# Performance work log

Measured on AMD Instinct MI355X. Metric: run time of the kernel, lower is better.

The kernel has to match this reference:

```python
import jax, jax.numpy as jnp
import numpy as np

WIDTH = 64
HEIGHT = 64
FEAT = 128
LAT = 64
NUM_SLOTS = 7


def pixel_coords(img_size):
    g = jnp.linspace(-1.0, 1.0, img_size)
    g1, g2 = jnp.meshgrid(g, g, indexing='ij')  # matches torch.meshgrid default
    return jnp.stack([g1, g2], axis=0)[None]  # (1, 2, S, S)


def clamp_pg(x, lo, hi):
    # clamp that preserves gradients (straight-through)
    return x + jax.lax.stop_gradient(jnp.clip(x, lo, hi) - x)


def setup_inputs() -> dict:
    key = jax.random.key(0)
    k0, k1, k2, k3 = jax.random.split(key, 4)
    bs = 64
    x = jax.random.normal(k0, (bs, FEAT, WIDTH, HEIGHT), jnp.float32)
    rand_pixel = jax.random.uniform(k1, (bs, 1, WIDTH, HEIGHT), jnp.float32)
    conv_w = jax.random.normal(k2, (LAT, FEAT), jnp.float32) / np.sqrt(FEAT)
    conv_b = jax.random.normal(k3, (LAT,), jnp.float32) * 0.01
    gate = jnp.asarray(0.5, jnp.float32)  # ScalarGate parameter (nonzero so c_f is non-degenerate)
    # laplacian kernel: sigma_init = 1 / (sqrt(num_slots) * log 2)
    log_sigma = jnp.asarray(np.log(1.0 / (np.sqrt(NUM_SLOTS) * np.log(2.0))), jnp.float32)
    return {'x': x, 'rand_pixel': rand_pixel, 'conv_w': conv_w, 'conv_b': conv_b,
            'gate': gate, 'log_sigma': log_sigma, 'num_cl_steps': 6}


def _forward(x, rand_pixel, conv_w, conv_b, gate, log_sigma, num_cl_steps):
    bs = x.shape[0]
    # SemiConv: gated 1x1 conv + fixed uv coordinate channels
    out = gate * (jnp.einsum('of,bfhw->bohw', conv_w, x) + conv_b[None, :, None, None])
    uv = jnp.concatenate([jnp.zeros((1, LAT - 2, WIDTH, HEIGHT), out.dtype),
                          pixel_coords(WIDTH).astype(out.dtype)], axis=1)
    c_f = out + uv                      # (bs, LAT, W, H)
    delta = out[:, -2:]                 # (bs, 2, W, H)
    sigma = jnp.exp(log_sigma)
    c_flat = c_f.reshape(bs, LAT, -1)   # (bs, LAT, W*H)
    b_idx = jnp.arange(bs)
    log_s0 = jnp.zeros((bs, 1, WIDTH, HEIGHT), c_f.dtype)

    def step(log_s, _):
        # interpolate-to-same-size is identity -> scope = exp(log_s)
        probs = (rand_pixel * jnp.exp(log_s)).reshape(bs, -1)
        idx = jnp.argmax(probs, axis=1)                 # (bs,)
        seed = c_flat[b_idx, :, idx]                    # (bs, LAT)
        diff = c_f - seed[:, :, None, None]
        dist = jnp.sqrt(clamp_pg((diff ** 2).sum(1), 1e-10, 1e10))  # euclidian (laplacian kernel)
        alpha = jnp.exp(-dist / sigma)[:, None]         # (bs, 1, W, H)
        alpha = clamp_pg(alpha, 0.01, 0.99)
        log_m = log_s + jnp.log(alpha)
        new_log_s = log_s + jnp.log1p(-alpha)
        return new_log_s, (log_m, new_log_s, seed)

    log_s_final, (log_m_steps, log_s_steps, seeds) = jax.lax.scan(
        step, log_s0, None, length=num_cl_steps)
    # log_m_k has num_cl_steps masks plus the final scope appended
    log_m_k = jnp.concatenate([log_m_steps, log_s_final[None]], axis=0)
    log_s_k = jnp.concatenate([log_s0[None], log_s_steps], axis=0)
    return log_m_k, log_s_k, c_f, delta, seeds


def reference(x, rand_pixel, conv_w, conv_b, gate, log_sigma, num_cl_steps):
    return _forward(x, rand_pixel, conv_w, conv_b, gate, log_sigma, num_cl_steps)
```

## Files before the change

kernel.cpp:

```cpp
#include <hip/hip_runtime.h>
#include <hip/hip_bf16.h>

#define NPIX 4096
#define FEAT 128
#define LAT 64
#define BS 64
#define NSTEPS 6

#define OFF_LOGM  0u
#define OFF_LOGS  1835008u
#define OFF_CF    3670016u
#define OFF_DELTA 20447232u
#define OFF_SEEDS 20971520u

typedef float f32x4 __attribute__((ext_vector_type(4)));
typedef short s16x8 __attribute__((ext_vector_type(8)));

__device__ __forceinline__ void amax_comb(float& bv, int& bi, float v, int i) {
    if (v > bv || (v == bv && i < bi)) { bv = v; bi = i; }
}

__device__ __forceinline__ short f2bf_rne(float r) {
    __hip_bfloat16 h = __float2bfloat16(r);
    return __builtin_bit_cast(short, h);
}

__device__ __forceinline__ void split2(float v, short& hi, short& lo) {
    unsigned u = __builtin_bit_cast(unsigned, v);
    hi = (short)(u >> 16);
    float hf = __builtin_bit_cast(float, u & 0xFFFF0000u);
    lo = f2bf_rne(v - hf);
}

__device__ __forceinline__ void transpose4(float4& v, int b) {
    float4 w;
    w.x = __shfl_xor(v.x, 1, 64); w.y = __shfl_xor(v.y, 1, 64);
    w.z = __shfl_xor(v.z, 1, 64); w.w = __shfl_xor(v.w, 1, 64);
    float4 u;
    if ((b & 1) == 0) u = make_float4(v.x, w.x, v.z, w.z);
    else              u = make_float4(w.y, v.y, w.w, v.w);
    float4 w2;
    w2.x = __shfl_xor(u.x, 2, 64); w2.y = __shfl_xor(u.y, 2, 64);
    w2.z = __shfl_xor(u.z, 2, 64); w2.w = __shfl_xor(u.w, 2, 64);
    if ((b & 2) == 0) v = make_float4(u.x, u.y, w2.x, w2.y);
    else              v = make_float4(w2.z, w2.w, u.z, u.w);
}

__global__ void prep_w(const float* __restrict__ w, const float* __restrict__ gate_p,
                       short* __restrict__ gwh, short* __restrict__ gwl)
{
    int i = blockIdx.x * 256 + threadIdx.x;
    float v = gate_p[0] * w[i];
    short h, l; split2(v, h, l);
    gwh[i] = h; gwl[i] = l;
}

__global__ __launch_bounds__(512, 2) void conv_mfma(
    const float* __restrict__ x, const float* __restrict__ rand_pixel,
    const float* __restrict__ bias, const float* __restrict__ gate_p,
    float* __restrict__ out,
    float* __restrict__ pval, int* __restrict__ pidx, int* __restrict__ cnt,
    const short* __restrict__ gwh, const short* __restrict__ gwl)
{
    __shared__ __align__(16) short Xhi[256][40];
    __shared__ __align__(16) short Xlo[256][40];
    __shared__ __align__(16) short Whi[64][132];
    __shared__ __align__(16) short Wlo[64][132];
    __shared__ float sbias[64];

    const int tid  = threadIdx.x;
    const int b    = blockIdx.x >> 4;
    const int tile = blockIdx.x & 15;
    const int p0   = tile * 256;
    const int lane = tid & 63;
    const int wv   = tid >> 6;
    const int l15  = lane & 15;
    const int lg   = lane >> 4;
    const int oh   = wv >> 2;
    const int pxq  = wv & 3;

    const int q  = tid >> 2;
    const int j  = tid & 3;
    const int P  = (q & 63) * 4;
    const int g0 = q >> 6;

    if (tile == 0 && tid < 8) cnt[b * 8 + tid] = 0;
    if (tid < 64) sbias[tid] = gate_p[0] * bias[tid];

    const float* xb = x + (size_t)b * FEAT * NPIX + p0;
    float4 v[4][4];
    #pragma unroll
    for (int kc = 0; kc < 4; ++kc)
        #pragma unroll
        for (int i = 0; i < 4; ++i) {
            int g = g0 + 2 * i;
            v[kc][i] = *(const float4*)(xb + (size_t)(kc * 32 + g * 4 + j) * NPIX + P);
        }

    {
        const int o = tid >> 3, c = (tid & 7) * 16;
        *(s16x8*)&Whi[o][c]     = *(const s16x8*)&gwh[o * 128 + c];
        *(s16x8*)&Whi[o][c + 8] = *(const s16x8*)&gwh[o * 128 + c + 8];
        *(s16x8*)&Wlo[o][c]     = *(const s16x8*)&gwl[o * 128 + c];
        *(s16x8*)&Wlo[o][c + 8] = *(const s16x8*)&gwl[o * 128 + c + 8];
    }

    #pragma unroll
    for (int i = 0; i < 4; ++i) {
        int g = g0 + 2 * i;
        float4 t = v[0][i]; transpose4(t, j);
        short h0, l0, h1, l1, h2, l2, h3, l3;
        split2(t.x, h0, l0); split2(t.y, h1, l1);
        split2(t.z, h2, l2); split2(t.w, h3, l3);
        *(short4*)&Xhi[P + j][g * 4] = make_short4(h0, h1, h2, h3);
        *(short4*)&Xlo[P + j][g * 4] = make_short4(l0, l1, l2, l3);
    }
    __syncthreads();

    f32x4 acc[2][4];
    #pragma unroll
    for (int og2 = 0; og2 < 2; ++og2)
        #pragma unroll
        for (int pg = 0; pg < 4; ++pg)
            acc[og2][pg] = (f32x4){0.f, 0.f, 0.f, 0.f};

    #pragma unroll
    for (int kc = 0; kc < 4; ++kc) {
        s16x8 Ah[2], Al[2];
        #pragma unroll
        for (int og2 = 0; og2 < 2; ++og2) {
            int o = oh * 32 + og2 * 16 + l15;
            Ah[og2] = *(const s16x8*)&Whi[o][kc * 32 + lg * 8];
            Al[og2] = *(const s16x8*)&Wlo[o][kc * 32 + lg * 8];
        }

        #pragma unroll
        for (int pg = 0; pg < 4; ++pg) {
            int pxl = pxq * 64 + pg * 16 + l15;
            s16x8 Bh = *(const s16x8*)&Xhi[pxl][lg * 8];
            s16x8 Bl = *(const s16x8*)&Xlo[pxl][lg * 8];
            #pragma unroll
            for (int og2 = 0; og2 < 2; ++og2) {
                acc[og2][pg] = __builtin_amdgcn_mfma_f32_16x16x32_bf16(Ah[og2], Bh, acc[og2][pg], 0, 0, 0);
                acc[og2][pg] = __builtin_amdgcn_mfma_f32_16x16x32_bf16(Ah[og2], Bl, acc[og2][pg], 0, 0, 0);
                acc[og2][pg] = __builtin_amdgcn_mfma_f32_16x16x32_bf16(Al[og2], Bh, acc[og2][pg], 0, 0, 0);
            }
        }

        if (kc < 3) {
            __syncthreads();
            #pragma unroll
            for (int i = 0; i < 4; ++i) {
                int g = g0 + 2 * i;
                float4 t = v[kc + 1][i]; transpose4(t, j);
                short h0, l0, h1, l1, h2, l2, h3, l3;
                split2(t.x, h0, l0); split2(t.y, h1, l1);
                split2(t.z, h2, l2); split2(t.w, h3, l3);
                *(short4*)&Xhi[P + j][g * 4] = make_short4(h0, h1, h2, h3);
                *(short4*)&Xlo[P + j][g * 4] = make_short4(l0, l1, l2, l3);
            }
            __syncthreads();
        }
    }

    float* cf = out + OFF_CF + (size_t)b * LAT * NPIX;
    #pragma unroll
    for (int og2 = 0; og2 < 2; ++og2) {
        #pragma unroll
        for (int pg = 0; pg < 4; ++pg) {
            #pragma unroll
            for (int r = 0; r < 4; ++r) {
                int o = oh * 32 + og2 * 16 + lg * 4 + r;
                int p = p0 + pxq * 64 + pg * 16 + l15;
                float vv = acc[og2][pg][r] + sbias[o];
                if (o == 62) {
                    out[OFF_DELTA + ((size_t)b * 2 + 0) * NPIX + p] = vv;
                    vv += (float)(-1.0 + 2.0 * (double)(p >> 6) / 63.0);
                } else if (o == 63) {
                    out[OFF_DELTA + ((size_t)b * 2 + 1) * NPIX + p] = vv;
                    vv += (float)(-1.0 + 2.0 * (double)(p & 63) / 63.0);
                }
                cf[(size_t)o * NPIX + p] = vv;
            }
        }
    }

    if (wv == 0) {
        *(float4*)(out + OFF_LOGS + (size_t)b * NPIX + p0 + lane * 4) =
            make_float4(0.f, 0.f, 0.f, 0.f);
        float4 rv = *(const float4*)(rand_pixel + (size_t)b * NPIX + p0 + lane * 4);
        int pb = p0 + lane * 4;
        float bv = rv.x; int bi = pb;
        if (rv.y > bv) { bv = rv.y; bi = pb + 1; }
        if (rv.z > bv) { bv = rv.z; bi = pb + 2; }
        if (rv.w > bv) { bv = rv.w; bi = pb + 3; }
        #pragma unroll
        for (int off = 32; off > 0; off >>= 1) {
            float ov = __shfl_down(bv, off, 64);
            int   oi = __shfl_down(bi, off, 64);
            amax_comb(bv, bi, ov, oi);
        }
        if (lane == 0) { pval[blockIdx.x] = bv; pidx[blockIdx.x] = bi; }
    }
}

#define REP16(OP) OP(0) OP(1) OP(2) OP(3) OP(4) OP(5) OP(6) OP(7) \
                  OP(8) OP(9) OP(10) OP(11) OP(12) OP(13) OP(14) OP(15)

__global__ __launch_bounds__(1024, 4) void steps_fused(
    const float* __restrict__ rand_pixel, const float* __restrict__ log_sigma_p,
    float* __restrict__ out, float* pv, int* pi, int* cnt)
{
    __shared__ float s_mv[16];
    __shared__ int   s_mi[16];
    __shared__ __align__(16) float s_seed[LAT];
    __shared__ float s_rv[16];
    __shared__ int   s_ri[16];

    const int tid  = threadIdx.x;
    const int b    = blockIdx.x >> 2;
    const int tile = blockIdx.x & 3;
    const int p    = tile * 1024 + tid;

    const float* cfb = out + OFF_CF + (size_t)b * LAT * NPIX;

#define DECLR(i) f32x4 r##i;
    REP16(DECLR)
#define LOADR(i) r##i = (f32x4){ cfb[(size_t)(4*i+0)*NPIX + p], cfb[(size_t)(4*i+1)*NPIX + p], \
                                 cfb[(size_t)(4*i+2)*NPIX + p], cfb[(size_t)(4*i+3)*NPIX + p] };
    REP16(LOADR)

    f32x4 aq = r0 * r0;
#define SQR(i) aq += r##i * r##i;
    SQR(1) SQR(2) SQR(3) SQR(4) SQR(5) SQR(6) SQR(7)
    SQR(8) SQR(9) SQR(10) SQR(11) SQR(12) SQR(13) SQR(14) SQR(15)
    const float cr2 = aq[0] + aq[1] + aq[2] + aq[3];

    const float rp    = rand_pixel[(size_t)b * NPIX + p];
    const float sigma = expf(log_sigma_p[0]);
    float ls = 0.f;

    #pragma unroll 1
    for (int s = 0; s < NSTEPS; ++s) {
        if (s > 0) {
            if (tid == 0) {
                while (__hip_atomic_load(&cnt[b * 8 + s], __ATOMIC_ACQUIRE,
                                         __HIP_MEMORY_SCOPE_AGENT) < 4)
                    __builtin_amdgcn_s_sleep(2);
            }
            __syncthreads();
        }
        const int nmerge = (s == 0) ? 16 : 4;
        if (tid < nmerge) {
            s_mv[tid] = __hip_atomic_load(&pv[(s * BS + b) * 16 + tid],
                                          __ATOMIC_RELAXED, __HIP_MEMORY_SCOPE_AGENT);
            s_mi[tid] = __hip_atomic_load(&pi[(s * BS + b) * 16 + tid],
                                          __ATOMIC_RELAXED, __HIP_MEMORY_SCOPE_AGENT);
        }
        __syncthreads();

        float bv = -1.0f; int bi = 0;
        for (int k = 0; k < nmerge; ++k) amax_comb(bv, bi, s_mv[k], s_mi[k]);

        if (tid < LAT) s_seed[tid] = cfb[(size_t)tid * NPIX + bi];
        __syncthreads();
        if (tile == 0 && tid < LAT)
            out[OFF_SEEDS + ((size_t)s * BS + b) * LAT + tid] = s_seed[tid];

        f32x4 dacc = (f32x4){0.f, 0.f, 0.f, 0.f};
        f32x4 sacc = (f32x4){0.f, 0.f, 0.f, 0.f};
#define DOT(i) { f32x4 sv = *(const f32x4*)&s_seed[4*i]; dacc += r##i * sv; sacc += sv * sv; }
        REP16(DOT)
        float dot = dacc[0] + dacc[1] + dacc[2] + dacc[3];
        float s2  = sacc[0] + sacc[1] + sacc[2] + sacc[3];
        float d2  = cr2 + s2 - 2.0f * dot;

        float dist  = sqrtf(fminf(fmaxf(d2, 1e-10f), 1e10f));
        float alpha = expf(-dist / sigma);
        alpha = fminf(fmaxf(alpha, 0.01f), 0.99f);
        float lm  = ls + logf(alpha);
        float lsn = ls + log1pf(-alpha);

        out[OFF_LOGM + ((size_t)s * BS + b) * NPIX + p]       = lm;
        out[OFF_LOGS + ((size_t)(s + 1) * BS + b) * NPIX + p] = lsn;
        ls = lsn;

        if (s == NSTEPS - 1) {
            out[OFF_LOGM + ((size_t)NSTEPS * BS + b) * NPIX + p] = lsn;
        } else {
            float prob = rp * expf(lsn);
            int   idx  = p;
            #pragma unroll
            for (int off = 32; off > 0; off >>= 1) {
                float ov = __shfl_down(prob, off, 64);
                int   oi = __shfl_down(idx, off, 64);
                amax_comb(prob, idx, ov, oi);
            }
            int lane = tid & 63, wid = tid >> 6;
            if (lane == 0) { s_rv[wid] = prob; s_ri[wid] = idx; }
            __syncthreads();
            if (tid == 0) {
                float fb = s_rv[0]; int fi = s_ri[0];
                #pragma unroll
                for (int k = 1; k < 16; ++k) amax_comb(fb, fi, s_rv[k], s_ri[k]);
                __hip_atomic_store(&pv[((s + 1) * BS + b) * 16 + tile], fb,
                                   __ATOMIC_RELAXED, __HIP_MEMORY_SCOPE_AGENT);
                __hip_atomic_store(&pi[((s + 1) * BS + b) * 16 + tile], fi,
                                   __ATOMIC_RELAXED, __HIP_MEMORY_SCOPE_AGENT);
                __hip_atomic_fetch_add(&cnt[b * 8 + s + 1], 1,
                                       __ATOMIC_RELEASE, __HIP_MEMORY_SCOPE_AGENT);
            }
        }
    }
}

__global__ __launch_bounds__(1024, 4) void step_kernel(
    const float* __restrict__ rand_pixel, const float* __restrict__ log_sigma_p,
    float* __restrict__ out, float* pv, int* pi, int step)
{
    __shared__ float s_mv[16];
    __shared__ int   s_mi[16];
    __shared__ __align__(16) float s_seed[LAT];
    __shared__ float s_rv[16];
    __shared__ int   s_ri[16];

    const int tid  = threadIdx.x;
    const int b    = blockIdx.x >> 2;
    const int tile = blockIdx.x & 3;
    const int p    = tile * 1024 + tid;

    const float* cfb = out + OFF_CF + (size_t)b * LAT * NPIX;

    const int nmerge = (step == 0) ? 16 : 4;
    if (tid < nmerge) { s_mv[tid] = pv[(step * BS + b) * 16 + tid];
                        s_mi[tid] = pi[(step * BS + b) * 16 + tid]; }
    __syncthreads();
    float bv = -1.0f; int bi = 0;
    for (int k = 0; k < nmerge; ++k) amax_comb(bv, bi, s_mv[k], s_mi[k]);

    if (tid < LAT) s_seed[tid] = cfb[(size_t)tid * NPIX + bi];
    __syncthreads();
    if (tile == 0 && tid < LAT)
        out[OFF_SEEDS + ((size_t)step * BS + b) * LAT + tid] = s_seed[tid];

    float d2 = 0.f;
    #pragma unroll
    for (int c = 0; c < LAT; ++c) {
        float d = cfb[(size_t)c * NPIX + p] - s_seed[c];
        d2 = fmaf(d, d, d2);
    }
    float dist  = sqrtf(fminf(fmaxf(d2, 1e-10f), 1e10f));
    float sigma = expf(log_sigma_p[0]);
    float alpha = expf(-dist / sigma);
    alpha = fminf(fmaxf(alpha, 0.01f), 0.99f);

    float ls  = out[OFF_LOGS + ((size_t)step * BS + b) * NPIX + p];
    float lm  = ls + logf(alpha);
    float lsn = ls + log1pf(-alpha);

    out[OFF_LOGM + ((size_t)step * BS + b) * NPIX + p]       = lm;
    out[OFF_LOGS + ((size_t)(step + 1) * BS + b) * NPIX + p] = lsn;
    if (step == NSTEPS - 1)
        out[OFF_LOGM + ((size_t)NSTEPS * BS + b) * NPIX + p] = lsn;

    if (step < NSTEPS - 1) {
        float prob = rand_pixel[(size_t)b * NPIX + p] * expf(lsn);
        int   idx  = p;
        #pragma unroll
        for (int off = 32; off > 0; off >>= 1) {
            float ov = __shfl_down(prob, off, 64);
            int   oi = __shfl_down(idx, off, 64);
            amax_comb(prob, idx, ov, oi);
        }
        int lane = tid & 63, wid = tid >> 6;
        if (lane == 0) { s_rv[wid] = prob; s_ri[wid] = idx; }
        __syncthreads();
        if (tid == 0) {
            float fb = s_rv[0]; int fi = s_ri[0];
            #pragma unroll
            for (int k = 1; k < 16; ++k) amax_comb(fb, fi, s_rv[k], s_ri[k]);
            pv[((step + 1) * BS + b) * 16 + tile] = fb;
            pi[((step + 1) * BS + b) * 16 + tile] = fi;
        }
    }
}

extern "C" void kernel_launch(void* const* d_in, const int* in_sizes, int n_in,
                              void* d_out, int out_size, void* d_ws, size_t ws_size,
                              hipStream_t stream) {
    const float* x          = (const float*)d_in[0];
    const float* rand_pixel = (const float*)d_in[1];
    const float* w          = (const float*)d_in[2];
    const float* bias       = (const float*)d_in[3];
    const float* gate       = (const float*)d_in[4];
    const float* log_sigma  = (const float*)d_in[5];

    float* out = (float*)d_out;
    float* pv  = (float*)d_ws;
    int*   pi  = (int*)((char*)d_ws + 24576);
    int*   cnt = (int*)((char*)d_ws + 49152);
    short* gwh = (short*)((char*)d_ws + 51200);
    short* gwl = (short*)((char*)d_ws + 67584);

    prep_w<<<32, 256, 0, stream>>>(w, gate, gwh, gwl);
    conv_mfma<<<1024, 512, 0, stream>>>(x, rand_pixel, bias, gate, out,
                                        pv, pi, cnt, gwh, gwl);

    const float* a0 = rand_pixel; const float* a1 = log_sigma; float* a2 = out;
    float* a3 = pv; int* a4 = pi; int* a5 = cnt;
    void* kp[6] = {(void*)&a0, (void*)&a1, (void*)&a2, (void*)&a3, (void*)&a4, (void*)&a5};
    hipError_t e = hipLaunchCooperativeKernel((const void*)steps_fused,
                                              dim3(256), dim3(1024), kp, 0, stream);
    if (e != hipSuccess) {
        for (int s = 0; s < NSTEPS; ++s)
            step_kernel<<<256, 1024, 0, stream>>>(rand_pixel, log_sigma, out, pv, pi, s);
    }
}
```

Measured before the change: 133.9 us.

## Load conv input straight into MFMA B-operand registers, drop LDS staging

The input activation tile is no longer staged through shared memory. Each wave now loads float4 chunks of x directly from global memory per K-chunk, transposes them across lanes with shuffles, and splits them into bf16 hi/lo B fragments in registers. This removes the X LDS buffers and the intra-loop barriers, and raises the launch-bounds occupancy hint from 2 to 4 blocks. The cost is that global loads are no longer issued all up front, so less latency is hidden, and lanes that share pixels may load overlapping data through cache.

```diff
diff --git a/kernel.cpp b/kernel.cpp
--- a/kernel.cpp
+++ b/kernel.cpp
@@ -55,15 +55,13 @@
     gwh[i] = h; gwl[i] = l;
 }
 
-__global__ __launch_bounds__(512, 2) void conv_mfma(
+__global__ __launch_bounds__(512, 4) void conv_mfma(
     const float* __restrict__ x, const float* __restrict__ rand_pixel,
     const float* __restrict__ bias, const float* __restrict__ gate_p,
     float* __restrict__ out,
     float* __restrict__ pval, int* __restrict__ pidx, int* __restrict__ cnt,
     const short* __restrict__ gwh, const short* __restrict__ gwl)
 {
-    __shared__ __align__(16) short Xhi[256][40];
-    __shared__ __align__(16) short Xlo[256][40];
     __shared__ __align__(16) short Whi[64][132];
     __shared__ __align__(16) short Wlo[64][132];
     __shared__ float sbias[64];
@@ -78,24 +76,10 @@
     const int lg   = lane >> 4;
     const int oh   = wv >> 2;
     const int pxq  = wv & 3;
-
-    const int q  = tid >> 2;
-    const int j  = tid & 3;
-    const int P  = (q & 63) * 4;
-    const int g0 = q >> 6;
+    const int j    = lane & 3;
 
     if (tile == 0 && tid < 8) cnt[b * 8 + tid] = 0;
     if (tid < 64) sbias[tid] = gate_p[0] * bias[tid];
-
-    const float* xb = x + (size_t)b * FEAT * NPIX + p0;
-    float4 v[4][4];
-    #pragma unroll
-    for (int kc = 0; kc < 4; ++kc)
-        #pragma unroll
-        for (int i = 0; i < 4; ++i) {
-            int g = g0 + 2 * i;
-            v[kc][i] = *(const float4*)(xb + (size_t)(kc * 32 + g * 4 + j) * NPIX + P);
-        }
 
     {
         const int o = tid >> 3, c = (tid & 7) * 16;
@@ -104,17 +88,6 @@
         *(s16x8*)&Wlo[o][c]     = *(const s16x8*)&gwl[o * 128 + c];
         *(s16x8*)&Wlo[o][c + 8] = *(const s16x8*)&gwl[o * 128 + c + 8];
     }
-
-    #pragma unroll
-    for (int i = 0; i < 4; ++i) {
-        int g = g0 + 2 * i;
-        float4 t = v[0][i]; transpose4(t, j);
-        short h0, l0, h1, l1, h2, l2, h3, l3;
-        split2(t.x, h0, l0); split2(t.y, h1, l1);
-        split2(t.z, h2, l2); split2(t.w, h3, l3);
-        *(short4*)&Xhi[P + j][g * 4] = make_short4(h0, h1, h2, h3);
-        *(short4*)&Xlo[P + j][g * 4] = make_short4(l0, l1, l2, l3);
-    }
     __syncthreads();
 
     f32x4 acc[2][4];
@@ -124,8 +97,18 @@
         for (int pg = 0; pg < 4; ++pg)
             acc[og2][pg] = (f32x4){0.f, 0.f, 0.f, 0.f};
 
+    const float* xb = x + (size_t)b * FEAT * NPIX + p0 + pxq * 64 + (l15 & ~3);
+
     #pragma unroll
     for (int kc = 0; kc < 4; ++kc) {
+        float4 t[4][2];
+        #pragma unroll
+        for (int pg = 0; pg < 4; ++pg) {
+            const float* xp = xb + (size_t)(kc * 32 + lg * 8 + j) * NPIX + pg * 16;
+            t[pg][0] = *(const float4*)(xp);
+            t[pg][1] = *(const float4*)(xp + (size_t)4 * NPIX);
+        }
+
         s16x8 Ah[2], Al[2];
         #pragma unroll
         for (int og2 = 0; og2 < 2; ++og2) {
@@ -136,30 +119,26 @@
 
         #pragma unroll
         for (int pg = 0; pg < 4; ++pg) {
-            int pxl = pxq * 64 + pg * 16 + l15;
-            s16x8 Bh = *(const s16x8*)&Xhi[pxl][lg * 8];
-            s16x8 Bl = *(const s16x8*)&Xlo[pxl][lg * 8];
+            float4 t0 = t[pg][0];
+            float4 t1 = t[pg][1];
+            transpose4(t0, j);
+            transpose4(t1, j);
+            s16x8 Bh, Bl;
+            short h, l;
+            split2(t0.x, h, l); Bh[0] = h; Bl[0] = l;
+            split2(t0.y, h, l); Bh[1] = h; Bl[1] = l;
+            split2(t0.z, h, l); Bh[2] = h; Bl[2] = l;
+            split2(t0.w, h, l); Bh[3] = h; Bl[3] = l;
+            split2(t1.x, h, l); Bh[4] = h; Bl[4] = l;
+            split2(t1.y, h, l); Bh[5] = h; Bl[5] = l;
+            split2(t1.z, h, l); Bh[6] = h; Bl[6] = l;
+            split2(t1.w, h, l); Bh[7] = h; Bl[7] = l;
             #pragma unroll
             for (int og2 = 0; og2 < 2; ++og2) {
                 acc[og2][pg] = __builtin_amdgcn_mfma_f32_16x16x32_bf16(Ah[og2], Bh, acc[og2][pg], 0, 0, 0);
                 acc[og2][pg] = __builtin_amdgcn_mfma_f32_16x16x32_bf16(Ah[og2], Bl, acc[og2][pg], 0, 0, 0);
                 acc[og2][pg] = __builtin_amdgcn_mfma_f32_16x16x32_bf16(Al[og2], Bh, acc[og2][pg], 0, 0, 0);
             }
-        }
-
-        if (kc < 3) {
-            __syncthreads();
-            #pragma unroll
-            for (int i = 0; i < 4; ++i) {
-                int g = g0 + 2 * i;
-                float4 t = v[kc + 1][i]; transpose4(t, j);
-                short h0, l0, h1, l1, h2, l2, h3, l3;
-                split2(t.x, h0, l0); split2(t.y, h1, l1);
-                split2(t.z, h2, l2); split2(t.w, h3, l3);
-                *(short4*)&Xhi[P + j][g * 4] = make_short4(h0, h1, h2, h3);
-                *(short4*)&Xlo[P + j][g * 4] = make_short4(l0, l1, l2, l3);
-            }
-            __syncthreads();
         }
     }
 
```

Result: slower. 138.0 us (+3.1%).
